# Kernel optimization log

Hardware: AMD Instinct MI355X
Metric: run time of the kernel (lower is better)

The kernel has to match this reference:

```python
import jax, jax.numpy as jnp
import numpy as np

N_POINTS = 1_200_000
MAX_POINTS = 10
MAX_VOXELS = 160_000


def setup_inputs() -> dict:
    key = jax.random.key(0)
    k1, k2, k3 = jax.random.split(key, 3)
    xy = jax.random.normal(k1, (N_POINTS, 2), dtype=jnp.float32) * 18.0
    z = jax.random.normal(k2, (N_POINTS, 1), dtype=jnp.float32) * 1.3 - 1.0
    feat = jax.random.normal(k3, (N_POINTS, 2), dtype=jnp.float32)
    points = jnp.concatenate([xy, z, feat], axis=1)
    return {
        'points': points,
        'voxel_size': jnp.array([0.075, 0.075, 0.2], dtype=jnp.float32),
        'coors_range': jnp.array([-54.0, -54.0, -5.0, 54.0, 54.0, 3.0], dtype=jnp.float32),
        'max_points': MAX_POINTS,
        'max_voxels': MAX_VOXELS,
    }


def reference(points, voxel_size, coors_range, max_points, max_voxels):
    """Deterministic hard voxelization (mmcv hard_voxelize semantics):
    - quantize points to integer voxel coords, drop out-of-range points
    - voxels are numbered in order of first point appearance
    - at most `max_points` points per voxel (first ones kept, in point order)
    - at most `max_voxels` voxels (first ones kept)
    Returns fixed-shape buffers plus voxel_num (original slices to voxel_num).
    """
    N, C = points.shape
    vmin = coors_range[:3]
    grid = jnp.round((coors_range[3:] - vmin) / voxel_size).astype(jnp.int32)  # (gx, gy, gz)

    c = jnp.floor((points[:, :3] - vmin) / voxel_size).astype(jnp.int32)  # [N,3] xyz voxel coords
    valid = jnp.all((c >= 0) & (c < grid), axis=1)

    gx, gy, gz = grid[0].astype(jnp.int64), grid[1].astype(jnp.int64), grid[2].astype(jnp.int64)
    lin = (c[:, 0].astype(jnp.int64) * gy + c[:, 1].astype(jnp.int64)) * gz + c[:, 2].astype(jnp.int64)
    total = gx * gy * gz
    lin = jnp.where(valid, lin, total)  # sentinel sorts last

    idx = jnp.arange(N, dtype=jnp.int64)
    # composite key: group by voxel, original point order within each voxel
    order = jnp.argsort(lin * N + idx)  # [N] stable grouping
    lin_s = lin[order]
    valid_s = valid[order]

    is_head = valid_s & jnp.concatenate([jnp.array([True]), lin_s[1:] != lin_s[:-1]])
    pos = jnp.arange(N, dtype=jnp.int32)
    head_pos = jax.lax.cummax(jnp.where(is_head, pos, -1))  # head position of each point's group
    slot = pos - head_pos  # slot within voxel (point order)

    # voxel id = rank of the group's first point among all group-head original indices
    head_orig = jnp.where(is_head, order, N)  # sentinel N for non-heads
    rank = jnp.argsort(jnp.argsort(head_orig)).astype(jnp.int32)  # heads -> 0..H-1 in first-occurrence order
    vox_id = rank[head_pos]  # [N] voxel id per sorted point

    keep = valid_s & (slot < max_points) & (vox_id < max_voxels)
    vid = jnp.where(keep, vox_id, max_voxels)  # dump row for dropped points
    slt = jnp.where(keep, slot, 0)
    vals = jnp.where(keep[:, None], points[order], 0.0)

    voxels = jnp.zeros((max_voxels + 1, max_points, C), dtype=points.dtype)
    voxels = voxels.at[vid, slt].add(vals)[:max_voxels]

    # coors in (z, y, x) order as in mmcv
    c_rev = c[order][:, ::-1]
    vid_h = jnp.where(is_head & (rank < max_voxels), rank, max_voxels)
    coors = jnp.zeros((max_voxels + 1, 3), dtype=jnp.int32)
    coors = coors.at[vid_h].set(jnp.where((vid_h < max_voxels)[:, None], c_rev, 0))[:max_voxels]

    cnt_idx = jnp.where(valid_s & (vox_id < max_voxels), vox_id, max_voxels)
    counts = jnp.zeros((max_voxels + 1,), dtype=jnp.int32).at[cnt_idx].add(1)[:max_voxels]
    num_points_per_voxel = jnp.minimum(counts, max_points)

    voxel_num = jnp.minimum(is_head.sum(dtype=jnp.int32), max_voxels)
    return voxels, coors, num_points_per_voxel, voxel_num
```

## Files before the change

kernel.cpp:

```cpp
#include <hip/hip_runtime.h>
#include <cstdint>

static constexpr int C     = 5;
static constexpr int MAXP  = 10;
static constexpr int MAXV  = 160000;
static constexpr int BLK   = 256;
static constexpr int RB    = 2048;
static constexpr int BCAP  = 1024;
static constexpr int EPT   = 8;
static constexpr int ELEMS = BLK * EPT;

static constexpr int VOX_OFF = 0;
static constexpr int CO_OFF  = MAXV * MAXP * C;
static constexpr int NPV_OFF = CO_OFF + MAXV * 3;
static constexpr int VN_OFF  = NPV_OFF + MAXV;

typedef unsigned long long u64;
static constexpr u64 BYTEMUL = 0x0101010101010101ull;

__device__ __forceinline__ int hashb(int k) {
    return (int)(((uint32_t)k * 2654435761u) >> 21);
}

__global__ void vx_prep(const float* __restrict__ pts, const float* __restrict__ vsz,
                        const float* __restrict__ crg, int* __restrict__ key0,
                        int* __restrict__ hist, u64* __restrict__ flags8,
                        float* __restrict__ out, int NP, int NP8) {
    __shared__ int sh[RB];
    int t = threadIdx.x, b = blockIdx.x;
    for (int d = t; d < RB; d += BLK) sh[d] = 0;
    float vx = vsz[0], vy = vsz[1], vz = vsz[2];
    float x0 = crg[0], y0 = crg[1], z0 = crg[2];
    int gx = (int)rintf((crg[3] - x0) / vx);
    int gy = (int)rintf((crg[4] - y0) / vy);
    int gz = (int)rintf((crg[5] - z0) / vz);
    __syncthreads();
    int base = b * ELEMS;
    #pragma unroll
    for (int r = 0; r < EPT; r++) {
        int i = base + r * BLK + t;
        if (i < NP) {
            float px = pts[i * C], py = pts[i * C + 1], pz = pts[i * C + 2];
            int cx = (int)floorf((px - x0) / vx);
            int cy = (int)floorf((py - y0) / vy);
            int cz = (int)floorf((pz - z0) / vz);
            bool valid = (cx >= 0) & (cx < gx) & (cy >= 0) & (cy < gy) & (cz >= 0) & (cz < gz);
            int k = (cx * gy + cy) * gz + cz;
            key0[i] = valid ? k : -1;
            if (valid) atomicAdd(&sh[hashb(k)], 1);
        }
    }
    __syncthreads();
    for (int d = t; d < RB; d += BLK) hist[b * RB + d] = sh[d];
    int tid = b * BLK + t, nth = gridDim.x * BLK;
    float4* out4 = (float4*)out;
    const float4 z4 = make_float4(0.f, 0.f, 0.f, 0.f);
    for (int i = tid; i < VN_OFF / 4; i += nth) out4[i] = z4;
    for (int i = tid; i < NP8; i += nth) flags8[i] = 0ull;
}

__global__ void vx_scanw(int* __restrict__ hist, int* __restrict__ dtot, int NB) {
    int t = threadIdx.x;
    int lane = t & 63;
    int d = blockIdx.x * 4 + (t >> 6);
    int carry = 0;
    for (int base = 0; base < NB; base += 64) {
        int b = base + lane;
        int v = (b < NB) ? hist[b * RB + d] : 0;
        int x = v;
        #pragma unroll
        for (int o = 1; o < 64; o <<= 1) {
            int y = __shfl_up(x, o, 64);
            if (lane >= o) x += y;
        }
        if (b < NB) hist[b * RB + d] = carry + x - v;
        carry += __shfl(x, 63, 64);
    }
    if (lane == 0) dtot[d] = carry;
}

__global__ void vx_scat(const int* __restrict__ key0, const int* __restrict__ hist,
                        const int* __restrict__ dtot, u64* __restrict__ pairA, int NP) {
    __shared__ int cnt[RB];
    int t = threadIdx.x, b = blockIdx.x;
    int lane = t & 63;
    if (t < 64) {
        int loc[32]; int run = 0;
        #pragma unroll
        for (int j = 0; j < 32; j++) { loc[j] = run; run += dtot[t * 32 + j]; }
        int tot = run;
        for (int o = 1; o < 64; o <<= 1) {
            int x = __shfl_up(tot, o, 64);
            if (lane >= o) tot += x;
        }
        int excl = tot - run;
        #pragma unroll
        for (int j = 0; j < 32; j++) cnt[t * 32 + j] = excl + loc[j];
    }
    __syncthreads();
    for (int d = t; d < RB; d += BLK) cnt[d] += hist[b * RB + d];
    __syncthreads();
    int base = b * ELEMS;
    #pragma unroll
    for (int r = 0; r < EPT; r++) {
        int i = base + r * BLK + t;
        if (i < NP) {
            int k = key0[i];
            if (k >= 0) {
                int pos = atomicAdd(&cnt[hashb(k)], 1);
                pairA[pos] = ((u64)(uint32_t)k << 32) | (uint32_t)i;
            }
        }
    }
}

__global__ void __launch_bounds__(512) vx_group(u64* __restrict__ pairA,
                                                const int* __restrict__ dtot,
                                                u64* __restrict__ flags8) {
    __shared__ int htab[BCAP];
    __shared__ int cnt[BCAP];
    __shared__ int seg[BCAP];
    __shared__ u64 sq[BCAP];
    __shared__ int swp[8];
    __shared__ int sb[2];
    int t = threadIdx.x, d = blockIdx.x;
    if (t < 64) {
        int acc = 0;
        for (int j = t; j < d; j += 64) acc += dtot[j];
        #pragma unroll
        for (int o = 32; o > 0; o >>= 1) acc += __shfl_down(acc, o, 64);
        if (t == 0) { sb[0] = acc; sb[1] = dtot[d]; }
    }
    for (int i = t; i < BCAP; i += 512) { htab[i] = -1; cnt[i] = 0; }
    __syncthreads();
    int start = sb[0], size = sb[1];
    if (size <= 0) return;
    if (size > BCAP) size = BCAP;
    bool a0 = t < size, a1 = t + 512 < size;
    u64 e0 = a0 ? pairA[start + t] : 0;
    u64 e1 = a1 ? pairA[start + 512 + t] : 0;
    int k0 = (int)(e0 >> 32), k1 = (int)(e1 >> 32);
    int s0 = 0, s1 = 0;
    if (a0) {
        s0 = (int)(((uint32_t)k0 * 0x85EBCA77u) >> 22);
        for (int it = 0; it < BCAP; ++it) {
            int old = atomicCAS(&htab[s0], -1, k0);
            if (old == -1 || old == k0) break;
            s0 = (s0 + 1) & (BCAP - 1);
        }
        atomicAdd(&cnt[s0], 1);
    }
    if (a1) {
        s1 = (int)(((uint32_t)k1 * 0x85EBCA77u) >> 22);
        for (int it = 0; it < BCAP; ++it) {
            int old = atomicCAS(&htab[s1], -1, k1);
            if (old == -1 || old == k1) break;
            s1 = (s1 + 1) & (BCAP - 1);
        }
        atomicAdd(&cnt[s1], 1);
    }
    __syncthreads();
    int c0 = cnt[2 * t], c1 = cnt[2 * t + 1];
    int v = c0 + c1;
    int lane = t & 63, wv = t >> 6;
    int x = v;
    #pragma unroll
    for (int o = 1; o < 64; o <<= 1) {
        int y = __shfl_up(x, o, 64);
        if (lane >= o) x += y;
    }
    if (lane == 63) swp[wv] = x;
    for (int i = t; i < BCAP; i += 512) htab[i] = 0;
    __syncthreads();
    if (t == 0) {
        int acc = 0;
        #pragma unroll
        for (int j = 0; j < 8; j++) { int tmp = swp[j]; swp[j] = acc; acc += tmp; }
    }
    __syncthreads();
    int excl = swp[wv] + x - v;
    seg[2 * t] = excl;
    seg[2 * t + 1] = excl + c0;
    __syncthreads();
    int st0 = 0, cn0 = 0, st1 = 0, cn1 = 0;
    if (a0) { st0 = seg[s0]; cn0 = cnt[s0]; sq[st0 + atomicAdd(&htab[s0], 1)] = e0; }
    if (a1) { st1 = seg[s1]; cn1 = cnt[s1]; sq[st1 + atomicAdd(&htab[s1], 1)] = e1; }
    __syncthreads();
    unsigned char* flags = (unsigned char*)flags8;
    if (a0) {
        uint32_t my = (uint32_t)e0;
        int r = 0;
        for (int q = st0; q < st0 + cn0; q++) r += ((uint32_t)sq[q] < my);
        pairA[start + st0 + r] = e0;
        if (r == 0) flags[my] = 1;
    }
    if (a1) {
        uint32_t my = (uint32_t)e1;
        int r = 0;
        for (int q = st1; q < st1 + cn1; q++) r += ((uint32_t)sq[q] < my);
        pairA[start + st1 + r] = e1;
        if (r == 0) flags[my] = 1;
    }
}

__global__ void vx_wpA(const u64* __restrict__ flags8, int* __restrict__ wsum, int NP8) {
    __shared__ int s[BLK];
    int t = threadIdx.x, i = blockIdx.x * BLK + t;
    u64 wv = (i < NP8) ? flags8[i] : 0ull;
    s[t] = (int)((wv * BYTEMUL) >> 56);
    __syncthreads();
    for (int o = BLK / 2; o > 0; o >>= 1) { if (t < o) s[t] += s[t + o]; __syncthreads(); }
    if (t == 0) wsum[blockIdx.x] = s[0];
}

__global__ void vx_wp2(const u64* __restrict__ flags8, const int* __restrict__ wsum,
                       int* __restrict__ wpfx, float* __restrict__ out_vnum, int NP8) {
    __shared__ int s[BLK];
    __shared__ int eS;
    int t = threadIdx.x, b = blockIdx.x;
    if (t < 64) {
        int acc = 0;
        for (int base = 0; base < b; base += 64) {
            int idx = base + t;
            int v = (idx < b) ? wsum[idx] : 0;
            #pragma unroll
            for (int o = 32; o > 0; o >>= 1) v += __shfl_down(v, o, 64);
            acc += v;
        }
        if (t == 0) eS = acc;
    }
    int i = b * BLK + t;
    u64 wv = (i < NP8) ? flags8[i] : 0ull;
    int v = (int)((wv * BYTEMUL) >> 56);
    s[t] = v;
    __syncthreads();
    for (int o = 1; o < BLK; o <<= 1) {
        int x = (t >= o) ? s[t - o] : 0; __syncthreads();
        s[t] += x; __syncthreads();
    }
    if (i < NP8) wpfx[i] = eS + s[t] - v;
    if (b == gridDim.x - 1 && t == BLK - 1) {
        int G = eS + s[t];
        out_vnum[0] = (float)(G < MAXV ? G : MAXV);
    }
}

__device__ __forceinline__ int vox_rank(const u64* flags8, const int* wpfx, int io) {
    int w = io >> 3, b8 = io & 7;
    u64 below = flags8[w] & ((1ull << (8 * b8)) - 1ull);
    return wpfx[w] + (int)((below * BYTEMUL) >> 56);
}

__global__ void vx_emit(const u64* __restrict__ pairA, const int* __restrict__ dtot,
                        const u64* __restrict__ flags8, const int* __restrict__ wpfx,
                        const float* __restrict__ pts, const float* __restrict__ vsz,
                        const float* __restrict__ crg, float* __restrict__ out) {
    __shared__ u64 sp[BCAP];
    __shared__ int gpos[BCAP + 1];
    __shared__ int s[BLK];
    __shared__ int sb[2];
    int t = threadIdx.x, d = blockIdx.x;
    if (t < 64) {
        int acc = 0;
        for (int j = t; j < d; j += 64) acc += dtot[j];
        #pragma unroll
        for (int o = 32; o > 0; o >>= 1) acc += __shfl_down(acc, o, 64);
        if (t == 0) { sb[0] = acc; sb[1] = dtot[d]; }
    }
    __syncthreads();
    int start = sb[0], size = sb[1];
    if (size <= 0) return;
    if (size > BCAP) size = BCAP;
    for (int i = t; i < size; i += BLK) sp[i] = pairA[start + i];
    __syncthreads();
    const int EL = BCAP / BLK;
    int i0 = t * EL;
    unsigned hbits = 0; int hcnt = 0;
    #pragma unroll
    for (int r = 0; r < EL; r++) {
        int i = i0 + r;
        if (i < size) {
            int k = (int)(sp[i] >> 32);
            int h = (i == 0) || (k != (int)(sp[i - 1] >> 32));
            hbits |= (unsigned)h << r;
            hcnt += h;
        }
    }
    s[t] = hcnt;
    __syncthreads();
    for (int o = 1; o < BLK; o <<= 1) {
        int x = (t >= o) ? s[t - o] : 0; __syncthreads();
        s[t] += x; __syncthreads();
    }
    int gbase = s[t] - hcnt;
    {
        int g = gbase;
        #pragma unroll
        for (int r = 0; r < EL; r++)
            if ((hbits >> r) & 1) gpos[g++] = i0 + r;
    }
    int NG = s[BLK - 1];
    if (t == 0) gpos[NG] = size;
    __syncthreads();
    int gyd = (int)rintf((crg[4] - crg[1]) / vsz[1]);
    int gzd = (int)rintf((crg[5] - crg[2]) / vsz[2]);
    int gg = gbase - 1;
    int cgg = -2, cvid = 0, cp0 = 0, cp1 = 0;
    #pragma unroll
    for (int r = 0; r < EL; r++) {
        int i = i0 + r;
        if (i >= size) break;
        int h = (hbits >> r) & 1;
        gg += h;
        u64 p = sp[i];
        int k = (int)(p >> 32);
        if (gg != cgg) {
            cgg = gg;
            cp0 = gpos[gg];
            cp1 = gpos[gg + 1];
            cvid = vox_rank(flags8, wpfx, (int)(sp[cp0] & 0xFFFFFFFFull));
        }
        if (cvid >= MAXV) continue;
        if (h) {
            int cz = k % gzd; int rr = k / gzd; int cy = rr % gyd; int cx = rr / gyd;
            out[CO_OFF + cvid * 3 + 0] = (float)cz;
            out[CO_OFF + cvid * 3 + 1] = (float)cy;
            out[CO_OFF + cvid * 3 + 2] = (float)cx;
            int gsz = cp1 - cp0;
            out[NPV_OFF + cvid] = (float)(gsz < MAXP ? gsz : MAXP);
        }
        int slot = i - cp0;
        if (slot >= MAXP) continue;
        int io = (int)(p & 0xFFFFFFFFull);
        const float* src = pts + io * C;
        float* dst = out + (cvid * MAXP + slot) * C;
        dst[0] = src[0]; dst[1] = src[1]; dst[2] = src[2]; dst[3] = src[3]; dst[4] = src[4];
    }
}

extern "C" void kernel_launch(void* const* d_in, const int* in_sizes, int n_in,
                              void* d_out, int out_size, void* d_ws, size_t ws_size,
                              hipStream_t stream) {
    if (!d_out || !d_ws || n_in < 3) return;
    const float* pts = (const float*)d_in[0];
    const float* vsz = (const float*)d_in[1];
    const float* crg = (const float*)d_in[2];
    if (!pts || !vsz || !crg) return;
    const int NP  = in_sizes[0] / C;
    if (NP <= 0) return;
    const int NB  = (NP + ELEMS - 1) / ELEMS;
    const int NP8 = (NP + 7) / 8;
    const int NWB = (NP8 + BLK - 1) / BLK;

    size_t need = (size_t)NP * 8ull
                + (size_t)NP * 4ull
                + (size_t)RB * NB * 4ull
                + (size_t)RB * 4ull
                + (size_t)NP8 * 8ull
                + (size_t)NP8 * 4ull
                + (size_t)NWB * 4ull + 64ull;
    if (ws_size < need) return;
    if ((size_t)out_size < (size_t)VN_OFF + 1) return;

    u64* pairA  = (u64*)d_ws;
    int* key0   = (int*)(pairA + NP);
    int* hist   = key0 + NP;
    int* dtot   = hist + (size_t)RB * NB;
    u64* flags8 = (u64*)(dtot + RB);
    int* wpfx   = (int*)(flags8 + NP8);
    int* wsum   = wpfx + NP8;
    float* out  = (float*)d_out;

    vx_prep<<<NB, BLK, 0, stream>>>(pts, vsz, crg, key0, hist, flags8, out, NP, NP8);
    vx_scanw<<<RB / 4, BLK, 0, stream>>>(hist, dtot, NB);
    vx_scat<<<NB, BLK, 0, stream>>>(key0, hist, dtot, pairA, NP);
    vx_group<<<RB, 512, 0, stream>>>(pairA, dtot, flags8);
    vx_wpA<<<NWB, BLK, 0, stream>>>(flags8, wsum, NP8);
    vx_wp2<<<NWB, BLK, 0, stream>>>(flags8, wsum, wpfx, out + VN_OFF, NP8);
    vx_emit<<<RB, BLK, 0, stream>>>(pairA, dtot, flags8, wpfx, pts, vsz, crg, out);
}
```

Baseline: 180.2 us.

## Emit per-point records in group pass and replace bucket emit with flat final pass

The group kernel now writes a 16-byte record per point (key, index, head index, slot and group size) instead of rewriting sorted pairs. The old per-bucket emit kernel is replaced by a flat per-point kernel that resolves the voxel id from the head and writes outputs directly. The output is no longer zeroed up front; only the used rows' tails and the region past the voxel count are zeroed, which avoids one full 32 MB memset pass. It skips the rank loop for singleton groups and adds a valid-point counter via atomics, at the cost of extra record traffic and redundant rank lookups per point.

```diff
diff --git a/kernel.cpp b/kernel.cpp
--- a/kernel.cpp
+++ b/kernel.cpp
@@ -25,10 +25,12 @@
 __global__ void vx_prep(const float* __restrict__ pts, const float* __restrict__ vsz,
                         const float* __restrict__ crg, int* __restrict__ key0,
                         int* __restrict__ hist, u64* __restrict__ flags8,
-                        float* __restrict__ out, int NP, int NP8) {
+                        int* __restrict__ ctrl, float* __restrict__ out,
+                        int NP, int NP8) {
     __shared__ int sh[RB];
     int t = threadIdx.x, b = blockIdx.x;
     for (int d = t; d < RB; d += BLK) sh[d] = 0;
+    if (b == 0 && t < 8) ctrl[t] = 0;
     float vx = vsz[0], vy = vsz[1], vz = vsz[2];
     float x0 = crg[0], y0 = crg[1], z0 = crg[2];
     int gx = (int)rintf((crg[3] - x0) / vx);
@@ -53,9 +55,10 @@
     __syncthreads();
     for (int d = t; d < RB; d += BLK) hist[b * RB + d] = sh[d];
     int tid = b * BLK + t, nth = gridDim.x * BLK;
-    float4* out4 = (float4*)out;
+    float4* co4 = (float4*)(out + CO_OFF);
     const float4 z4 = make_float4(0.f, 0.f, 0.f, 0.f);
-    for (int i = tid; i < VN_OFF / 4; i += nth) out4[i] = z4;
+    const int nco4 = (VN_OFF - CO_OFF) / 4;
+    for (int i = tid; i < nco4; i += nth) co4[i] = z4;
     for (int i = tid; i < NP8; i += nth) flags8[i] = 0ull;
 }
 
@@ -80,10 +83,13 @@
 }
 
 __global__ void vx_scat(const int* __restrict__ key0, const int* __restrict__ hist,
-                        const int* __restrict__ dtot, u64* __restrict__ pairA, int NP) {
+                        const int* __restrict__ dtot, u64* __restrict__ pairA,
+                        int* __restrict__ ctrl, int NP) {
     __shared__ int cnt[RB];
+    __shared__ int svld;
     int t = threadIdx.x, b = blockIdx.x;
     int lane = t & 63;
+    if (t == 0) svld = 0;
     if (t < 64) {
         int loc[32]; int run = 0;
         #pragma unroll
@@ -101,6 +107,7 @@
     for (int d = t; d < RB; d += BLK) cnt[d] += hist[b * RB + d];
     __syncthreads();
     int base = b * ELEMS;
+    int myv = 0;
     #pragma unroll
     for (int r = 0; r < EPT; r++) {
         int i = base + r * BLK + t;
@@ -109,14 +116,19 @@
             if (k >= 0) {
                 int pos = atomicAdd(&cnt[hashb(k)], 1);
                 pairA[pos] = ((u64)(uint32_t)k << 32) | (uint32_t)i;
+                myv++;
             }
         }
     }
-}
-
-__global__ void __launch_bounds__(512) vx_group(u64* __restrict__ pairA,
+    atomicAdd(&svld, myv);
+    __syncthreads();
+    if (t == 0) atomicAdd(&ctrl[1], svld);
+}
+
+__global__ void __launch_bounds__(512) vx_group(const u64* __restrict__ pairA,
                                                 const int* __restrict__ dtot,
-                                                u64* __restrict__ flags8) {
+                                                u64* __restrict__ flags8,
+                                                uint4* __restrict__ recs) {
     __shared__ int htab[BCAP];
     __shared__ int cnt[BCAP];
     __shared__ int seg[BCAP];
@@ -183,23 +195,35 @@
     seg[2 * t + 1] = excl + c0;
     __syncthreads();
     int st0 = 0, cn0 = 0, st1 = 0, cn1 = 0;
-    if (a0) { st0 = seg[s0]; cn0 = cnt[s0]; sq[st0 + atomicAdd(&htab[s0], 1)] = e0; }
-    if (a1) { st1 = seg[s1]; cn1 = cnt[s1]; sq[st1 + atomicAdd(&htab[s1], 1)] = e1; }
+    if (a0) { st0 = seg[s0]; cn0 = cnt[s0]; if (cn0 > 1) sq[st0 + atomicAdd(&htab[s0], 1)] = e0; }
+    if (a1) { st1 = seg[s1]; cn1 = cnt[s1]; if (cn1 > 1) sq[st1 + atomicAdd(&htab[s1], 1)] = e1; }
+    __syncthreads();
+    int r0 = 0, r1 = 0;
+    if (a0 && cn0 > 1) {
+        uint32_t my = (uint32_t)e0;
+        for (int q = st0; q < st0 + cn0; q++) r0 += ((uint32_t)sq[q] < my);
+        if (r0 == 0) htab[s0] = (int)my;
+    }
+    if (a1 && cn1 > 1) {
+        uint32_t my = (uint32_t)e1;
+        for (int q = st1; q < st1 + cn1; q++) r1 += ((uint32_t)sq[q] < my);
+        if (r1 == 0) htab[s1] = (int)my;
+    }
     __syncthreads();
     unsigned char* flags = (unsigned char*)flags8;
     if (a0) {
         uint32_t my = (uint32_t)e0;
-        int r = 0;
-        for (int q = st0; q < st0 + cn0; q++) r += ((uint32_t)sq[q] < my);
-        pairA[start + st0 + r] = e0;
-        if (r == 0) flags[my] = 1;
+        uint32_t head = (cn0 > 1) ? (uint32_t)htab[s0] : my;
+        if (r0 == 0) flags[my] = 1;
+        recs[start + st0 + r0] =
+            make_uint4((uint32_t)k0, my, head, (uint32_t)r0 | ((uint32_t)cn0 << 16));
     }
     if (a1) {
         uint32_t my = (uint32_t)e1;
-        int r = 0;
-        for (int q = st1; q < st1 + cn1; q++) r += ((uint32_t)sq[q] < my);
-        pairA[start + st1 + r] = e1;
-        if (r == 0) flags[my] = 1;
+        uint32_t head = (cn1 > 1) ? (uint32_t)htab[s1] : my;
+        if (r1 == 0) flags[my] = 1;
+        recs[start + st1 + r1] =
+            make_uint4((uint32_t)k1, my, head, (uint32_t)r1 | ((uint32_t)cn1 << 16));
     }
 }
 
@@ -214,7 +238,8 @@
 }
 
 __global__ void vx_wp2(const u64* __restrict__ flags8, const int* __restrict__ wsum,
-                       int* __restrict__ wpfx, float* __restrict__ out_vnum, int NP8) {
+                       int* __restrict__ wpfx, int* __restrict__ ctrl,
+                       float* __restrict__ out_vnum, int NP8) {
     __shared__ int s[BLK];
     __shared__ int eS;
     int t = threadIdx.x, b = blockIdx.x;
@@ -241,7 +266,9 @@
     if (i < NP8) wpfx[i] = eS + s[t] - v;
     if (b == gridDim.x - 1 && t == BLK - 1) {
         int G = eS + s[t];
-        out_vnum[0] = (float)(G < MAXV ? G : MAXV);
+        int Gk = G < MAXV ? G : MAXV;
+        ctrl[0] = Gk;
+        out_vnum[0] = (float)Gk;
     }
 }
 
@@ -251,90 +278,48 @@
     return wpfx[w] + (int)((below * BYTEMUL) >> 56);
 }
 
-__global__ void vx_emit(const u64* __restrict__ pairA, const int* __restrict__ dtot,
-                        const u64* __restrict__ flags8, const int* __restrict__ wpfx,
-                        const float* __restrict__ pts, const float* __restrict__ vsz,
-                        const float* __restrict__ crg, float* __restrict__ out) {
-    __shared__ u64 sp[BCAP];
-    __shared__ int gpos[BCAP + 1];
-    __shared__ int s[BLK];
-    __shared__ int sb[2];
-    int t = threadIdx.x, d = blockIdx.x;
-    if (t < 64) {
-        int acc = 0;
-        for (int j = t; j < d; j += 64) acc += dtot[j];
-        #pragma unroll
-        for (int o = 32; o > 0; o >>= 1) acc += __shfl_down(acc, o, 64);
-        if (t == 0) { sb[0] = acc; sb[1] = dtot[d]; }
-    }
-    __syncthreads();
-    int start = sb[0], size = sb[1];
-    if (size <= 0) return;
-    if (size > BCAP) size = BCAP;
-    for (int i = t; i < size; i += BLK) sp[i] = pairA[start + i];
-    __syncthreads();
-    const int EL = BCAP / BLK;
-    int i0 = t * EL;
-    unsigned hbits = 0; int hcnt = 0;
-    #pragma unroll
-    for (int r = 0; r < EL; r++) {
-        int i = i0 + r;
-        if (i < size) {
-            int k = (int)(sp[i] >> 32);
-            int h = (i == 0) || (k != (int)(sp[i - 1] >> 32));
-            hbits |= (unsigned)h << r;
-            hcnt += h;
-        }
-    }
-    s[t] = hcnt;
-    __syncthreads();
-    for (int o = 1; o < BLK; o <<= 1) {
-        int x = (t >= o) ? s[t - o] : 0; __syncthreads();
-        s[t] += x; __syncthreads();
-    }
-    int gbase = s[t] - hcnt;
-    {
-        int g = gbase;
-        #pragma unroll
-        for (int r = 0; r < EL; r++)
-            if ((hbits >> r) & 1) gpos[g++] = i0 + r;
-    }
-    int NG = s[BLK - 1];
-    if (t == 0) gpos[NG] = size;
-    __syncthreads();
+__global__ void vx_final(const uint4* __restrict__ recs, const u64* __restrict__ flags8,
+                         const int* __restrict__ wpfx, const int* __restrict__ ctrl,
+                         const float* __restrict__ pts, const float* __restrict__ vsz,
+                         const float* __restrict__ crg, float* __restrict__ out, int NP) {
+    int t = threadIdx.x, b = blockIdx.x;
+    int nval = ctrl[1], Gk = ctrl[0];
     int gyd = (int)rintf((crg[4] - crg[1]) / vsz[1]);
     int gzd = (int)rintf((crg[5] - crg[2]) / vsz[2]);
-    int gg = gbase - 1;
-    int cgg = -2, cvid = 0, cp0 = 0, cp1 = 0;
+    int base = b * ELEMS;
     #pragma unroll
-    for (int r = 0; r < EL; r++) {
-        int i = i0 + r;
-        if (i >= size) break;
-        int h = (hbits >> r) & 1;
-        gg += h;
-        u64 p = sp[i];
-        int k = (int)(p >> 32);
-        if (gg != cgg) {
-            cgg = gg;
-            cp0 = gpos[gg];
-            cp1 = gpos[gg + 1];
-            cvid = vox_rank(flags8, wpfx, (int)(sp[cp0] & 0xFFFFFFFFull));
-        }
-        if (cvid >= MAXV) continue;
-        if (h) {
+    for (int r = 0; r < EPT; r++) {
+        int i = base + r * BLK + t;
+        if (i >= nval) continue;
+        uint4 rec = recs[i];
+        int k = (int)rec.x;
+        uint32_t my = rec.y, head = rec.z;
+        int slot = (int)(rec.w & 0xFFFFu);
+        int gsz  = (int)(rec.w >> 16);
+        if (slot >= MAXP || head >= (uint32_t)NP || my >= (uint32_t)NP) continue;
+        int vid = vox_rank(flags8, wpfx, (int)head);
+        if (vid >= MAXV) continue;
+        const float* src = pts + my * C;
+        float* dst = out + (vid * MAXP + slot) * C;
+        dst[0] = src[0]; dst[1] = src[1]; dst[2] = src[2]; dst[3] = src[3]; dst[4] = src[4];
+        if (slot == 0) {
             int cz = k % gzd; int rr = k / gzd; int cy = rr % gyd; int cx = rr / gyd;
-            out[CO_OFF + cvid * 3 + 0] = (float)cz;
-            out[CO_OFF + cvid * 3 + 1] = (float)cy;
-            out[CO_OFF + cvid * 3 + 2] = (float)cx;
-            int gsz = cp1 - cp0;
-            out[NPV_OFF + cvid] = (float)(gsz < MAXP ? gsz : MAXP);
-        }
-        int slot = i - cp0;
-        if (slot >= MAXP) continue;
-        int io = (int)(p & 0xFFFFFFFFull);
-        const float* src = pts + io * C;
-        float* dst = out + (cvid * MAXP + slot) * C;
-        dst[0] = src[0]; dst[1] = src[1]; dst[2] = src[2]; dst[3] = src[3]; dst[4] = src[4];
+            out[CO_OFF + vid * 3 + 0] = (float)cz;
+            out[CO_OFF + vid * 3 + 1] = (float)cy;
+            out[CO_OFF + vid * 3 + 2] = (float)cx;
+            int np = gsz < MAXP ? gsz : MAXP;
+            out[NPV_OFF + vid] = (float)np;
+            float* rowz = out + (vid * MAXP + np) * C;
+            int nz = (MAXP - np) * C;
+            for (int z = 0; z < nz; z++) rowz[z] = 0.f;
+        }
+    }
+    int nz2 = (MAXV - Gk) * (MAXP * C) / 2;
+    if (nz2 > 0) {
+        float2* z2 = (float2*)(out + Gk * MAXP * C);
+        const float2 zz = make_float2(0.f, 0.f);
+        int tid = b * BLK + t, nth = gridDim.x * BLK;
+        for (int i = tid; i < nz2; i += nth) z2[i] = zz;
     }
 }
 
@@ -353,6 +338,7 @@
     const int NWB = (NP8 + BLK - 1) / BLK;
 
     size_t need = (size_t)NP * 8ull
+                + (size_t)NP * 16ull
                 + (size_t)NP * 4ull
                 + (size_t)RB * NB * 4ull
                 + (size_t)RB * 4ull
@@ -362,20 +348,22 @@
     if (ws_size < need) return;
     if ((size_t)out_size < (size_t)VN_OFF + 1) return;
 
-    u64* pairA  = (u64*)d_ws;
-    int* key0   = (int*)(pairA + NP);
-    int* hist   = key0 + NP;
-    int* dtot   = hist + (size_t)RB * NB;
-    u64* flags8 = (u64*)(dtot + RB);
-    int* wpfx   = (int*)(flags8 + NP8);
-    int* wsum   = wpfx + NP8;
-    float* out  = (float*)d_out;
-
-    vx_prep<<<NB, BLK, 0, stream>>>(pts, vsz, crg, key0, hist, flags8, out, NP, NP8);
+    u64*   pairA  = (u64*)d_ws;
+    uint4* recs   = (uint4*)(pairA + NP);
+    int*   key0   = (int*)(recs + NP);
+    int*   hist   = key0 + NP;
+    int*   dtot   = hist + (size_t)RB * NB;
+    u64*   flags8 = (u64*)(dtot + RB);
+    int*   wpfx   = (int*)(flags8 + NP8);
+    int*   wsum   = wpfx + NP8;
+    int*   ctrl   = wsum + NWB;
+    float* out    = (float*)d_out;
+
+    vx_prep<<<NB, BLK, 0, stream>>>(pts, vsz, crg, key0, hist, flags8, ctrl, out, NP, NP8);
     vx_scanw<<<RB / 4, BLK, 0, stream>>>(hist, dtot, NB);
-    vx_scat<<<NB, BLK, 0, stream>>>(key0, hist, dtot, pairA, NP);
-    vx_group<<<RB, 512, 0, stream>>>(pairA, dtot, flags8);
+    vx_scat<<<NB, BLK, 0, stream>>>(key0, hist, dtot, pairA, ctrl, NP);
+    vx_group<<<RB, 512, 0, stream>>>(pairA, dtot, flags8, recs);
     vx_wpA<<<NWB, BLK, 0, stream>>>(flags8, wsum, NP8);
-    vx_wp2<<<NWB, BLK, 0, stream>>>(flags8, wsum, wpfx, out + VN_OFF, NP8);
-    vx_emit<<<RB, BLK, 0, stream>>>(pairA, dtot, flags8, wpfx, pts, vsz, crg, out);
-}
+    vx_wp2<<<NWB, BLK, 0, stream>>>(flags8, wsum, wpfx, ctrl, out + VN_OFF, NP8);
+    vx_final<<<NB, BLK, 0, stream>>>(recs, flags8, wpfx, ctrl, pts, vsz, crg, out, NP);
+}
```

After: 203.0 us. +12.7%, slower.
